# Kernel optimization log

Hardware: AMD Instinct MI355X
Metric: run time of the kernel (lower is better)

Reference implementation:

```python
import jax, jax.numpy as jnp
import numpy as np

D = 1024
H = 16
HD = D // H
T = 2048
B = 2
EPS = 1e-6


def rmsnorm(x, w):
    xf = x.astype(jnp.float32)
    n = xf * jax.lax.rsqrt(jnp.mean(xf * xf, axis=-1, keepdims=True) + EPS)
    return n.astype(x.dtype) * w


def setup_inputs() -> dict:
    key = jax.random.key(0)
    ks = jax.random.split(key, 12)
    s_in = 1.0 / np.sqrt(D)
    s_h = 1.0 / np.sqrt(HD * H)
    s_ff = 1.0 / np.sqrt(4 * D)
    return {
        "x": jax.random.normal(ks[0], (B, T, D), jnp.float32),
        "wq": jax.random.normal(ks[1], (H, D, HD), jnp.float32) * s_in,
        "wk": jax.random.normal(ks[2], (H, D, HD), jnp.float32) * s_in,
        "wv": jax.random.normal(ks[3], (H, D, HD), jnp.float32) * s_in,
        "w_proj": jax.random.normal(ks[4], (D, D), jnp.float32) * s_h,
        "b_proj": jax.random.normal(ks[5], (D,), jnp.float32) * 0.01,
        "w1": jax.random.normal(ks[6], (D, 8 * D), jnp.float32) * s_in,
        "b1": jax.random.normal(ks[7], (8 * D,), jnp.float32) * 0.01,
        "w2": jax.random.normal(ks[8], (4 * D, D), jnp.float32) * s_ff,
        "b2": jax.random.normal(ks[9], (D,), jnp.float32) * 0.01,
        "g1": jnp.ones((D,), jnp.float32),
        "g2": jnp.ones((D,), jnp.float32),
    }


def reference(x, wq, wk, wv, w_proj, b_proj, w1, b1, w2, b2, g1, g2):
    # --- attention sub-block ---
    xn = rmsnorm(x, g1)
    q = jnp.einsum("btd,hde->bhte", xn, wq)  # [B,H,T,HD]
    k = jnp.einsum("btd,hde->bhte", xn, wk)
    v = jnp.einsum("btd,hde->bhte", xn, wv)
    scores = jnp.einsum("bhte,bhse->bhts", q, k) * (HD ** -0.5)
    causal = jnp.tril(jnp.ones((T, T), bool))
    scores = jnp.where(causal, scores, -jnp.inf)
    attn = jax.nn.softmax(scores, axis=-1)
    o = jnp.einsum("bhts,bhse->bhte", attn, v)  # [B,H,T,HD]
    o = o.transpose(0, 2, 1, 3).reshape(B, T, H * HD)  # concat heads
    x = x + o @ w_proj + b_proj
    # --- GLU FFN sub-block ---
    xn2 = rmsnorm(x, g2)
    h = xn2 @ w1 + b1  # [B,T,8D]
    a, b = jnp.split(h, 2, axis=-1)
    glu = a * jax.nn.sigmoid(b)  # [B,T,4D]
    x = x + glu @ w2 + b2
    return x
```

## Files before the change

kernel.cpp:

```cpp
#include <hip/hip_runtime.h>


typedef __attribute__((ext_vector_type(4))) float f32x4;
typedef __attribute__((ext_vector_type(8))) short short8;

typedef __attribute__((address_space(1))) const void gvoid;
typedef __attribute__((address_space(3))) void lvoid;

static __device__ __forceinline__ void gl_lds16(const void* g, void* l) {
  __builtin_amdgcn_global_load_lds((gvoid*)g, (lvoid*)l, 16, 0, 0);
}

static __device__ __forceinline__ unsigned short f2bf(float f) {
  union { float f; unsigned u; } v; v.f = f;
  unsigned r = v.u + 0x7fffu + ((v.u >> 16) & 1u);
  return (unsigned short)(r >> 16);
}
static __device__ __forceinline__ float to_f32(float v) { return v; }
static __device__ __forceinline__ float to_f32(unsigned short v) {
  union { unsigned u; float f; } x; x.u = ((unsigned)v) << 16; return x.f;
}

static __device__ __forceinline__ f32x4 mfma16(short8 a, short8 b, f32x4 c) {
  return __builtin_amdgcn_mfma_f32_16x16x32_bf16(a, b, c, 0, 0, 0);
}

template <typename Tin>
__global__ __launch_bounds__(256) void transpose_cvt(
    const Tin* __restrict__ in, unsigned short* __restrict__ out,
    int in_ld, long in_bstride, int out_ld, long out_bstride)
{
  __shared__ float tile[64][65];
  const Tin* inp = in + (long)blockIdx.z * in_bstride;
  unsigned short* outp = out + (long)blockIdx.z * out_bstride;
  int r0 = blockIdx.y * 64, c0 = blockIdx.x * 64;
  int tx = threadIdx.x & 63, ty = threadIdx.x >> 6;
#pragma unroll
  for (int i = ty; i < 64; i += 4)
    tile[i][tx] = to_f32(inp[(long)(r0 + i) * in_ld + (c0 + tx)]);
  __syncthreads();
#pragma unroll
  for (int i = ty; i < 64; i += 4)
    outp[(long)(c0 + i) * out_ld + (r0 + tx)] = f2bf(tile[tx][i]);
}

__global__ __launch_bounds__(256) void rmsnorm_k(
    const float* __restrict__ x, const float* __restrict__ g,
    unsigned short* __restrict__ out)
{
  int row = blockIdx.x;
  int t = threadIdx.x;
  float4 v = ((const float4*)(x + (long)row * 1024))[t];
  float ss = v.x * v.x + v.y * v.y + v.z * v.z + v.w * v.w;
#pragma unroll
  for (int ofs = 32; ofs; ofs >>= 1) ss += __shfl_down(ss, ofs);
  __shared__ float red[4];
  if ((t & 63) == 0) red[t >> 6] = ss;
  __syncthreads();
  float sc = rsqrtf((red[0] + red[1] + red[2] + red[3]) * (1.0f / 1024.0f) + 1e-6f);
  float4 gv = ((const float4*)g)[t];
  ushort4 o4;
  o4.x = f2bf(v.x * sc * gv.x); o4.y = f2bf(v.y * sc * gv.y);
  o4.z = f2bf(v.z * sc * gv.z); o4.w = f2bf(v.w * sc * gv.w);
  ((ushort4*)(out + (long)row * 1024))[t] = o4;
}

template <int EPI, int WM_, int WN_, bool GLUB, bool DBUF>
__global__ __launch_bounds__(256, 2) void gemm_bt(
    const unsigned short* __restrict__ A, const unsigned short* __restrict__ Bt,
    unsigned short* __restrict__ outb, float* __restrict__ outf,
    const float* __restrict__ res, const float* __restrict__ bias,
    int K, int lda, int ldbt, int ldout)
{
  constexpr int FM = 128 / (16 * WM_);
  constexpr int FN = 128 / (16 * WN_);
  constexpr int NBUF = DBUF ? 2 : 1;
  __shared__ alignas(16) unsigned short Asm_[NBUF * 128 * 64];
  __shared__ alignas(16) unsigned short Bsm_[NBUF * 128 * 64];
  const int tid = threadIdx.x, lane = tid & 63, wave = tid >> 6;
  const int lr = lane & 15, lg = lane >> 4;
  const int wr = wave / WN_, wc = wave % WN_;
  const int m0 = blockIdx.y * 128;

  f32x4 acc[FM][FN];
#pragma unroll
  for (int mi = 0; mi < FM; mi++)
#pragma unroll
    for (int ni = 0; ni < FN; ni++) acc[mi][ni] = f32x4{0.f, 0.f, 0.f, 0.f};

  int arow[4], au[4];
  long brow[4];
#pragma unroll
  for (int i = 0; i < 4; i++) {
    int U = tid + 256 * i;
    arow[i] = U >> 3;
    au[i] = ((U & 7) ^ (arow[i] & 7)) * 8;
    if (GLUB)
      brow[i] = (arow[i] < 64) ? (long)(blockIdx.x * 64 + arow[i])
                               : (long)(4096 + blockIdx.x * 64 + arow[i] - 64);
    else
      brow[i] = (long)blockIdx.x * 128 + arow[i];
  }

  auto stage = [&](int buf, int k0) {
#pragma unroll
    for (int i = 0; i < 4; i++) {
      gl_lds16(A + (long)(m0 + arow[i]) * lda + k0 + au[i],
               (char*)Asm_ + (buf * 1024 + wave * 64 + 256 * i) * 16);
      gl_lds16(Bt + brow[i] * ldbt + k0 + au[i],
               (char*)Bsm_ + (buf * 1024 + wave * 64 + 256 * i) * 16);
    }
  };

  if constexpr (DBUF) {
    stage(0, 0);
    __syncthreads();
  }

  for (int k0 = 0; k0 < K; k0 += 64) {
    int cur;
    if constexpr (DBUF) {
      cur = (k0 >> 6) & 1;
      if (k0 + 64 < K) stage(cur ^ 1, k0 + 64);
    } else {
      cur = 0;
      stage(0, k0);
      __syncthreads();
    }
    const char* ab = (const char*)Asm_ + cur * 16384;
    const char* bb = (const char*)Bsm_ + cur * 16384;

    short8 af[FM][2], bfr[FN][2];
#pragma unroll
    for (int mi = 0; mi < FM; mi++) {
      int row = wr * 16 * FM + mi * 16 + lr;
#pragma unroll
      for (int kk = 0; kk < 2; kk++) {
        int off = row * 128 + (((kk * 4 + lg) ^ (row & 7)) & 7) * 16;
        af[mi][kk] = *(const short8*)(ab + off);
      }
    }
#pragma unroll
    for (int ni = 0; ni < FN; ni++) {
      int row = wc * 16 * FN + ni * 16 + lr;
#pragma unroll
      for (int kk = 0; kk < 2; kk++) {
        int off = row * 128 + (((kk * 4 + lg) ^ (row & 7)) & 7) * 16;
        bfr[ni][kk] = *(const short8*)(bb + off);
      }
    }
#pragma unroll
    for (int kk = 0; kk < 2; kk++)
#pragma unroll
      for (int mi = 0; mi < FM; mi++)
#pragma unroll
        for (int ni = 0; ni < FN; ni++)
          acc[mi][ni] = mfma16(af[mi][kk], bfr[ni][kk], acc[mi][ni]);
    __syncthreads();
  }

  const int rb = m0 + wr * 16 * FM + 4 * lg;
  if constexpr (EPI == 0) {
#pragma unroll
    for (int mi = 0; mi < FM; mi++)
#pragma unroll
      for (int ni = 0; ni < FN; ni++) {
        int col = blockIdx.x * 128 + wc * 16 * FN + ni * 16 + lr;
#pragma unroll
        for (int r = 0; r < 4; r++)
          outb[(long)(rb + mi * 16 + r) * ldout + col] = f2bf(acc[mi][ni][r]);
      }
  } else if constexpr (EPI == 1) {
#pragma unroll
    for (int mi = 0; mi < FM; mi++)
#pragma unroll
      for (int ni = 0; ni < FN; ni++) {
        int col = blockIdx.x * 128 + wc * 16 * FN + ni * 16 + lr;
        float bv = bias[col];
#pragma unroll
        for (int r = 0; r < 4; r++) {
          long idx = (long)(rb + mi * 16 + r) * ldout + col;
          outf[idx] = acc[mi][ni][r] + res[idx] + bv;
        }
      }
  } else {
#pragma unroll
    for (int mi = 0; mi < FM; mi++)
#pragma unroll
      for (int ni = 0; ni < FN / 2; ni++) {
        int col = blockIdx.x * 64 + ni * 16 + lr;
        float ba = bias[col], bb2 = bias[4096 + col];
#pragma unroll
        for (int r = 0; r < 4; r++) {
          float a = acc[mi][ni][r] + ba;
          float b = acc[mi][ni + FN / 2][r] + bb2;
          float s = 1.0f / (1.0f + __expf(-b));
          outb[(long)(rb + mi * 16 + r) * ldout + col] = f2bf(a * s);
        }
      }
  }
}

__global__ __launch_bounds__(256, 2) void attn_k(
    const unsigned short* __restrict__ qkv, const unsigned short* __restrict__ vt,
    unsigned short* __restrict__ o)
{
  __shared__ alignas(16) unsigned short Ksm[2 * 128 * 64];
  __shared__ alignas(16) unsigned short Vsm[2 * 64 * 128];
  __shared__ alignas(16) unsigned short Psm[4][16 * 128];
  const int tid = threadIdx.x, lane = tid & 63, wave = tid >> 6;
  const int lr = lane & 15, lg = lane >> 4;
  const int bh = blockIdx.y, b = bh >> 4, h = bh & 15;
  const int ia = blockIdx.x;
  const int tA0 = ia * 64, tB0 = (31 - ia) * 64;
  const int nchA = (ia + 2) >> 1, nchB = (33 - ia) >> 1;
  const float NEGINF = -__builtin_inff();

  short8 qfA[2], qfB[2];
  {
    const unsigned short* qp =
        qkv + (long)(b * 2048 + tA0 + wave * 16 + lr) * 3072 + h * 64 + lg * 8;
    qfA[0] = *(const short8*)qp;  qfA[1] = *(const short8*)(qp + 32);
    qp = qkv + (long)(b * 2048 + tB0 + wave * 16 + lr) * 3072 + h * 64 + lg * 8;
    qfB[0] = *(const short8*)qp;  qfB[1] = *(const short8*)(qp + 32);
  }
  f32x4 oA[4], oB[4];
#pragma unroll
  for (int n = 0; n < 4; n++) { oA[n] = f32x4{0,0,0,0}; oB[n] = f32x4{0,0,0,0}; }
  float mA = NEGINF, lA = 0.f, mB = NEGINF, lB = 0.f;

  const long kbase = (long)(b * 2048) * 3072 + 1024 + h * 64;
  const long vbase = (long)bh * 64 * 2048;

  auto stage = [&](int buf, int c) {
    const int s0 = c * 128;
#pragma unroll
    for (int i = 0; i < 4; i++) {
      int U = tid + 256 * i;
      int kr = U >> 3, ku = (U ^ kr) & 7;
      gl_lds16(qkv + kbase + (long)(s0 + kr) * 3072 + ku * 8,
               (char*)Ksm + (buf * 1024 + wave * 64 + 256 * i) * 16);
      int vr = U >> 4, vu = (U & 8) | ((U ^ vr) & 7);
      gl_lds16(vt + vbase + (long)vr * 2048 + s0 + vu * 8,
               (char*)Vsm + (buf * 1024 + wave * 64 + 256 * i) * 16);
    }
  };

  char* pb = (char*)&Psm[wave][0];

  auto process = [&](const short8* qf, f32x4* o_acc, float& m, float& l,
                     const char* kb, const char* vb, int s0, int qg, bool diag) {
    f32x4 s[8];
#pragma unroll
    for (int n = 0; n < 8; n++) s[n] = f32x4{0.f, 0.f, 0.f, 0.f};
    __builtin_amdgcn_s_setprio(1);
#pragma unroll
    for (int n = 0; n < 8; n++) {
      int row = n * 16 + lr;
#pragma unroll
      for (int kk = 0; kk < 2; kk++) {
        int off = row * 128 + (((kk * 4 + lg) ^ row) & 7) * 16;
        short8 kf = *(const short8*)(kb + off);
        s[n] = mfma16(kf, qf[kk], s[n]);
      }
    }
    __builtin_amdgcn_s_setprio(0);
#pragma unroll
    for (int n = 0; n < 8; n++)
#pragma unroll
      for (int r = 0; r < 4; r++) {
        float v = s[n][r] * 0.125f;
        if (diag && (s0 + n * 16 + 4 * lg + r > qg)) v = NEGINF;
        s[n][r] = v;
      }
    float t[8];
#pragma unroll
    for (int n = 0; n < 8; n++)
      t[n] = fmaxf(fmaxf(s[n][0], s[n][1]), fmaxf(s[n][2], s[n][3]));
    float mx = fmaxf(fmaxf(fmaxf(t[0], t[1]), fmaxf(t[2], t[3])),
                     fmaxf(fmaxf(t[4], t[5]), fmaxf(t[6], t[7])));
    mx = fmaxf(mx, __shfl_xor(mx, 16));
    mx = fmaxf(mx, __shfl_xor(mx, 32));
    if (!__all(mx <= m + 8.0f)) {
      float mn = fmaxf(m, mx);
      float alpha = __expf(m - mn);
      m = mn;
      l *= alpha;
#pragma unroll
      for (int r = 0; r < 4; r++) {
        float ar = __shfl(alpha, 4 * lg + r);
#pragma unroll
        for (int n = 0; n < 4; n++) o_acc[n][r] *= ar;
      }
    }
    float sum = 0.f;
#pragma unroll
    for (int n = 0; n < 8; n++)
#pragma unroll
      for (int r = 0; r < 4; r++) {
        float p = __expf(s[n][r] - m);
        s[n][r] = p;
        sum += p;
      }
    sum += __shfl_xor(sum, 16);
    sum += __shfl_xor(sum, 32);
    l += sum;
#pragma unroll
    for (int n = 0; n < 8; n++) {
      unsigned lo = (unsigned)f2bf(s[n][0]) | ((unsigned)f2bf(s[n][1]) << 16);
      unsigned hi = (unsigned)f2bf(s[n][2]) | ((unsigned)f2bf(s[n][3]) << 16);
      int u = 2 * n + (lg >> 1);
      int su = (u & 8) | ((u ^ lr) & 7);
      *(uint2*)(pb + lr * 256 + su * 16 + 8 * (lg & 1)) = uint2{lo, hi};
    }
    asm volatile("s_waitcnt lgkmcnt(0)" ::: "memory");
    __builtin_amdgcn_sched_barrier(0);
    short8 pa[4];
#pragma unroll
    for (int ks = 0; ks < 4; ks++) {
      int u = 4 * ks + lg;
      int su = (u & 8) | ((u ^ lr) & 7);
      pa[ks] = *(const short8*)(pb + lr * 256 + su * 16);
    }
    __builtin_amdgcn_s_setprio(1);
#pragma unroll
    for (int n = 0; n < 4; n++) {
      int row = n * 16 + lr;
#pragma unroll
      for (int ks = 0; ks < 4; ks++) {
        int u = 4 * ks + lg;
        int su = (u & 8) | ((u ^ row) & 7);
        short8 vf = *(const short8*)(vb + row * 256 + su * 16);
        o_acc[n] = mfma16(pa[ks], vf, o_acc[n]);
      }
    }
    __builtin_amdgcn_s_setprio(0);
  };

  stage(0, 0);
  __syncthreads();

  const int qgA = tA0 + wave * 16 + lr, qgB = tB0 + wave * 16 + lr;
  for (int c = 0; c < nchB; c++) {
    if (c + 1 < nchB) stage((c + 1) & 1, c + 1);
    const char* kb = (const char*)Ksm + (c & 1) * 16384;
    const char* vb = (const char*)Vsm + (c & 1) * 16384;
    const int s0 = c * 128;
    if (c < nchA) process(qfA, oA, mA, lA, kb, vb, s0, qgA, c == nchA - 1);
    process(qfB, oB, mB, lB, kb, vb, s0, qgB, c == nchB - 1);
    __syncthreads();
  }

  auto finish = [&](const f32x4* o_acc, float l, int t0) {
#pragma unroll
    for (int r = 0; r < 4; r++) {
      float inv = 1.0f / __shfl(l, 4 * lg + r);
      int trow = t0 + wave * 16 + 4 * lg + r;
#pragma unroll
      for (int n = 0; n < 4; n++)
        o[(long)(b * 2048 + trow) * 1024 + h * 64 + n * 16 + lr] =
            f2bf(o_acc[n][r] * inv);
    }
  };
  finish(oA, lA, tA0);
  finish(oB, lB, tB0);
}

extern "C" void kernel_launch(void* const* d_in, const int* in_sizes, int n_in,
                              void* d_out, int out_size, void* d_ws, size_t ws_size,
                              hipStream_t stream) {
  const float* x     = (const float*)d_in[0];
  const float* wq    = (const float*)d_in[1];
  const float* wk    = (const float*)d_in[2];
  const float* wv    = (const float*)d_in[3];
  const float* wproj = (const float*)d_in[4];
  const float* bproj = (const float*)d_in[5];
  const float* w1    = (const float*)d_in[6];
  const float* b1    = (const float*)d_in[7];
  const float* w2    = (const float*)d_in[8];
  const float* b2    = (const float*)d_in[9];
  const float* g1    = (const float*)d_in[10];
  const float* g2    = (const float*)d_in[11];
  (void)in_sizes; (void)n_in; (void)out_size; (void)ws_size;

  char* ws = (char*)d_ws;
  unsigned short* wt_qkv = (unsigned short*)(ws);
  unsigned short* wpt    = (unsigned short*)(ws + (6ul << 20));
  unsigned short* w1t    = (unsigned short*)(ws + (8ul << 20));
  unsigned short* w2t    = (unsigned short*)(ws + (24ul << 20));
  unsigned short* xn     = (unsigned short*)(ws + (32ul << 20));
  unsigned short* qkv    = (unsigned short*)(ws + (40ul << 20));
  unsigned short* vt     = (unsigned short*)(ws + (64ul << 20));
  unsigned short* glu    = (unsigned short*)(ws + (40ul << 20));
  unsigned short* obuf   = (unsigned short*)(ws + (72ul << 20));
  float*          x1     = (float*)(ws + (80ul << 20));
  float* outf = (float*)d_out;

  transpose_cvt<float><<<dim3(1, 16, 16), 256, 0, stream>>>(
      wq, wt_qkv, 64, (long)1024 * 64, 1024, (long)64 * 1024);
  transpose_cvt<float><<<dim3(1, 16, 16), 256, 0, stream>>>(
      wk, wt_qkv + 1024ul * 1024, 64, (long)1024 * 64, 1024, (long)64 * 1024);
  transpose_cvt<float><<<dim3(1, 16, 16), 256, 0, stream>>>(
      wv, wt_qkv + 2048ul * 1024, 64, (long)1024 * 64, 1024, (long)64 * 1024);
  transpose_cvt<float><<<dim3(16, 16, 1), 256, 0, stream>>>(
      wproj, wpt, 1024, 0, 1024, 0);
  transpose_cvt<float><<<dim3(128, 16, 1), 256, 0, stream>>>(
      w1, w1t, 8192, 0, 1024, 0);
  transpose_cvt<float><<<dim3(16, 64, 1), 256, 0, stream>>>(
      w2, w2t, 1024, 0, 4096, 0);

  rmsnorm_k<<<4096, 256, 0, stream>>>(x, g1, xn);

  gemm_bt<0, 2, 2, false, false><<<dim3(24, 32), 256, 0, stream>>>(
      xn, wt_qkv, qkv, nullptr, nullptr, nullptr, 1024, 1024, 1024, 3072);

  transpose_cvt<unsigned short><<<dim3(1, 32, 16), 256, 0, stream>>>(
      qkv + 2048, vt, 3072, 64, 2048, (long)64 * 2048);
  transpose_cvt<unsigned short><<<dim3(1, 32, 16), 256, 0, stream>>>(
      qkv + 2048ul * 3072 + 2048, vt + 16ul * 64 * 2048, 3072, 64, 2048, (long)64 * 2048);

  attn_k<<<dim3(16, 32), 256, 0, stream>>>(qkv, vt, obuf);

  gemm_bt<1, 2, 2, false, true><<<dim3(8, 32), 256, 0, stream>>>(
      obuf, wpt, nullptr, x1, x, bproj, 1024, 1024, 1024, 1024);

  rmsnorm_k<<<4096, 256, 0, stream>>>(x1, g2, xn);

  gemm_bt<2, 4, 1, true, false><<<dim3(64, 32), 256, 0, stream>>>(
      xn, w1t, glu, nullptr, nullptr, b1, 1024, 1024, 1024, 4096);

  gemm_bt<1, 2, 2, false, true><<<dim3(8, 32), 256, 0, stream>>>(
      glu, w2t, nullptr, outf, x1, b2, 4096, 4096, 4096, 1024);
}
```

Before: 312.8 us.

## Replace GEMM staging with two-deep async LDS pipeline and vmcnt waits

Every GEMM now runs a two-stage global-to-LDS prefetch pipeline. The next tile is issued right after the barrier that ends compute, and partial s_waitcnt vmcnt(8) lets the following tile's loads stay in flight, replacing full __syncthreads drains. Wave priority is also raised around the MFMA block. The QKV and GLU GEMMs, which were single-buffered, now use double the LDS, which may lower occupancy. The vmcnt count assumes exactly 8 outstanding loads per stage.

```diff
diff --git a/kernel.cpp b/kernel.cpp
--- a/kernel.cpp
+++ b/kernel.cpp
@@ -65,7 +65,7 @@
   ((ushort4*)(out + (long)row * 1024))[t] = o4;
 }
 
-template <int EPI, int WM_, int WN_, bool GLUB, bool DBUF>
+template <int EPI, int WM_, int WN_, bool GLUB>
 __global__ __launch_bounds__(256, 2) void gemm_bt(
     const unsigned short* __restrict__ A, const unsigned short* __restrict__ Bt,
     unsigned short* __restrict__ outb, float* __restrict__ outf,
@@ -74,9 +74,8 @@
 {
   constexpr int FM = 128 / (16 * WM_);
   constexpr int FN = 128 / (16 * WN_);
-  constexpr int NBUF = DBUF ? 2 : 1;
-  __shared__ alignas(16) unsigned short Asm_[NBUF * 128 * 64];
-  __shared__ alignas(16) unsigned short Bsm_[NBUF * 128 * 64];
+  __shared__ alignas(16) unsigned short Asm_[2 * 128 * 64];
+  __shared__ alignas(16) unsigned short Bsm_[2 * 128 * 64];
   const int tid = threadIdx.x, lane = tid & 63, wave = tid >> 6;
   const int lr = lane & 15, lg = lane >> 4;
   const int wr = wave / WN_, wc = wave % WN_;
@@ -112,21 +111,16 @@
     }
   };
 
-  if constexpr (DBUF) {
-    stage(0, 0);
-    __syncthreads();
-  }
-
-  for (int k0 = 0; k0 < K; k0 += 64) {
-    int cur;
-    if constexpr (DBUF) {
-      cur = (k0 >> 6) & 1;
-      if (k0 + 64 < K) stage(cur ^ 1, k0 + 64);
-    } else {
-      cur = 0;
-      stage(0, k0);
-      __syncthreads();
-    }
+  stage(0, 0);
+  if (K > 64) stage(1, 64);
+
+  int it = 0;
+  for (int k0 = 0; k0 < K; k0 += 64, it++) {
+    if (k0 + 64 < K) asm volatile("s_waitcnt vmcnt(8)" ::: "memory");
+    else             asm volatile("s_waitcnt vmcnt(0)" ::: "memory");
+    __builtin_amdgcn_s_barrier();
+
+    const int cur = it & 1;
     const char* ab = (const char*)Asm_ + cur * 16384;
     const char* bb = (const char*)Bsm_ + cur * 16384;
 
@@ -149,6 +143,7 @@
         bfr[ni][kk] = *(const short8*)(bb + off);
       }
     }
+    __builtin_amdgcn_s_setprio(1);
 #pragma unroll
     for (int kk = 0; kk < 2; kk++)
 #pragma unroll
@@ -156,7 +151,10 @@
 #pragma unroll
         for (int ni = 0; ni < FN; ni++)
           acc[mi][ni] = mfma16(af[mi][kk], bfr[ni][kk], acc[mi][ni]);
-    __syncthreads();
+    __builtin_amdgcn_s_setprio(0);
+
+    __builtin_amdgcn_s_barrier();
+    if (k0 + 128 < K) stage(cur, k0 + 128);
   }
 
   const int rb = m0 + wr * 16 * FM + 4 * lg;
@@ -411,7 +409,7 @@
 
   rmsnorm_k<<<4096, 256, 0, stream>>>(x, g1, xn);
 
-  gemm_bt<0, 2, 2, false, false><<<dim3(24, 32), 256, 0, stream>>>(
+  gemm_bt<0, 2, 2, false><<<dim3(24, 32), 256, 0, stream>>>(
       xn, wt_qkv, qkv, nullptr, nullptr, nullptr, 1024, 1024, 1024, 3072);
 
   transpose_cvt<unsigned short><<<dim3(1, 32, 16), 256, 0, stream>>>(
@@ -421,14 +419,14 @@
 
   attn_k<<<dim3(16, 32), 256, 0, stream>>>(qkv, vt, obuf);
 
-  gemm_bt<1, 2, 2, false, true><<<dim3(8, 32), 256, 0, stream>>>(
+  gemm_bt<1, 2, 2, false><<<dim3(8, 32), 256, 0, stream>>>(
       obuf, wpt, nullptr, x1, x, bproj, 1024, 1024, 1024, 1024);
 
   rmsnorm_k<<<4096, 256, 0, stream>>>(x1, g2, xn);
 
-  gemm_bt<2, 4, 1, true, false><<<dim3(64, 32), 256, 0, stream>>>(
+  gemm_bt<2, 4, 1, true><<<dim3(64, 32), 256, 0, stream>>>(
       xn, w1t, glu, nullptr, nullptr, b1, 1024, 1024, 1024, 4096);
 
-  gemm_bt<1, 2, 2, false, true><<<dim3(8, 32), 256, 0, stream>>>(
+  gemm_bt<1, 2, 2, false><<<dim3(8, 32), 256, 0, stream>>>(
       glu, w2t, nullptr, outf, x1, b2, 4096, 4096, 4096, 1024);
 }
```

Result: no change. 313.3 us (+0.1%).
